# Performance work log

Hardware: AMD Instinct MI355X
Metric: run time of the kernel (lower is better)

The kernel has to match this reference:

```python
import jax, jax.numpy as jnp
import numpy as np

T, B, C, H, W = 4, 8, 256, 16, 16
HEADS = 8
N = H * W
TN = T * N
DH = C // HEADS
DECAY = 0.25

# STE quantizer: fwd round(clamp(x,0,1)); bwd passes grad only where 0<=x<=1
@jax.custom_vjp
def quant1(x):
    return jnp.round(jnp.clip(x, 0.0, 1.0))

def _q_fwd(x):
    return quant1(x), x

def _q_bwd(x, g):
    return (jnp.where((x < 0) | (x > 1), 0.0, g),)

quant1.defvjp(_q_fwd, _q_bwd)

def lif(x):
    # x: [T, ...]; sequential LIF membrane decay + quantize over leading (time) axis
    def step(carry, xt):
        mem_old, spike = carry
        mem = (mem_old - jax.lax.stop_gradient(spike) * 0.5) * DECAY + xt
        s = quant1(mem)
        return (mem, s), s
    z = jnp.zeros_like(x[0])
    _, out = jax.lax.scan(step, (z, z), x)
    return out

def bn1d(x, gamma, beta, mean, var):
    # eval-mode BatchNorm1d over channel axis 1 of [B, Ch, L]
    inv = jax.lax.rsqrt(var + 1e-5)
    return (x - mean[None, :, None]) * (gamma * inv)[None, :, None] + beta[None, :, None]

def _rel_pos_index():
    coords = np.stack(np.meshgrid(np.arange(T), np.arange(H), np.arange(W), indexing='ij'))  # [3,T,H,W]
    cf = coords.reshape(3, -1)                      # [3, TN]
    rc = (cf[:, :, None] - cf[:, None, :]).transpose(1, 2, 0).copy()  # [TN, TN, 3]
    rc[:, :, 0] += T - 1
    rc[:, :, 1] += H - 1
    rc[:, :, 2] += W - 1
    rc[:, :, 0] *= (2 * H - 1) * (2 * W - 1)
    rc[:, :, 1] *= (2 * W - 1)
    return rc.sum(-1)                               # [TN, TN] ints

def _mask():
    m = np.ones((TN, TN), np.float32)
    for t in range(T - 1):
        m[t * N:(t + 1) * N, (t + 1) * N:] = 0.0
    return m

_RPI = jnp.asarray(_rel_pos_index().reshape(-1))
_MASK = jnp.asarray(_mask())


def setup_inputs() -> dict:
    key = jax.random.key(0)
    ks = jax.random.split(key, 13)
    bias_rows = (2 * T - 1) * (2 * H - 1) * (2 * W - 1)
    return {
        'x': jax.random.normal(ks[0], (T, B, C, H, W), jnp.float32),
        'w_qkv': jax.random.normal(ks[1], (3 * C, C), jnp.float32) * 0.05,
        'qkv_gamma': jax.random.uniform(ks[2], (3 * C,), jnp.float32, 0.5, 1.5),
        'qkv_beta': jax.random.normal(ks[3], (3 * C,), jnp.float32) * 0.1,
        'qkv_mean': jax.random.normal(ks[4], (3 * C,), jnp.float32) * 0.1,
        'qkv_var': jax.random.uniform(ks[5], (3 * C,), jnp.float32, 0.5, 1.5),
        'bias_table': jax.random.normal(ks[6], (bias_rows, HEADS), jnp.float32) * 0.02,
        'w_proj': jax.random.normal(ks[7], (C, C), jnp.float32) * 0.05,
        'b_proj': jax.random.normal(ks[8], (C,), jnp.float32) * 0.02,
        'proj_gamma': jax.random.uniform(ks[9], (C,), jnp.float32, 0.5, 1.5),
        'proj_beta': jax.random.normal(ks[10], (C,), jnp.float32) * 0.1,
        'proj_mean': jax.random.normal(ks[11], (C,), jnp.float32) * 0.1,
        'proj_var': jax.random.uniform(ks[12], (C,), jnp.float32, 0.5, 1.5),
    }


def reference(x, w_qkv, qkv_gamma, qkv_beta, qkv_mean, qkv_var, bias_table,
              w_proj, b_proj, proj_gamma, proj_beta, proj_mean, proj_var):
    # flatten spatial, then raw reshape [T,B,C,N] -> [B,C,T*N] (as in torch source)
    xf = x.reshape(T, B, C, N).reshape(B, C, T * N)
    # 1x1 conv == channel matmul, then eval BN
    qkv = jnp.einsum('oc,bcl->bol', w_qkv, xf)
    qkv = bn1d(qkv, qkv_gamma, qkv_beta, qkv_mean, qkv_var)
    qkv = qkv.reshape(B, 3 * C, T, N).transpose(2, 0, 1, 3)  # [T,B,3C,N]
    qkv = lif(qkv).transpose(1, 0, 3, 2)                      # [B,T,N,3C]
    q, k, v = jnp.split(qkv, 3, axis=-1)                      # each [B,T,N,C]

    def to_heads(z):  # b t n (h d) -> b h (t n) d
        return z.reshape(B, T, N, HEADS, DH).transpose(0, 3, 1, 2, 4).reshape(B, HEADS, TN, DH)
    q, k, v = map(to_heads, (q, k, v))

    bias = bias_table[_RPI].reshape(TN, TN, HEADS).transpose(2, 0, 1)  # [h,TN,TN]
    attn = jnp.einsum('bhnd,bhmd->bhnm', q, k) + bias[None]
    attn = attn * _MASK[None, None]                                     # block upper-triangle mask
    o = jnp.einsum('bhnm,bhmd->bhnd', attn, v) * 0.125                  # [B,h,TN,d]

    o = o.transpose(0, 2, 1, 3).reshape(B, TN, C).reshape(B, T, N, C).transpose(1, 0, 3, 2)  # [T,B,C,N]
    o = lif(o)
    o = o.transpose(1, 2, 0, 3).reshape(B, C, T * N)          # [B,C,TN]
    o = jnp.einsum('oc,bcl->bol', w_proj, o) + b_proj[None, :, None]
    o = bn1d(o, proj_gamma, proj_beta, proj_mean, proj_var)
    o = o.reshape(B, C, T, N).transpose(2, 0, 1, 3).reshape(T, B, C, H, W)
    return lif(o)
```

## Files before the change

### kernel.cpp

```cpp
#include <hip/hip_runtime.h>
#include <stdint.h>
#include <math.h>

constexpr int T_ = 4;
constexpr int B_ = 8;
constexpr int C_ = 256;
constexpr int N_ = 256;
constexpr int TN_ = 1024;
constexpr int NH_ = 8;
constexpr int O3_ = 768;
constexpr int BIAS_ROWS_ = 6727;
constexpr int BCOL_P_ = 6784;

__device__ __constant__ int TI_OF[10] = {0,1,1,2,2,2,3,3,3,3};
__device__ __constant__ int TJ_OF[10] = {0,0,1,0,1,2,0,1,2,3};

__device__ __forceinline__ float quant1f(float m) {
    return rintf(fminf(fmaxf(m, 0.0f), 1.0f));
}

__global__ __launch_bounds__(256) void k0_bcol(
    const float* __restrict__ bias_table, float* __restrict__ bcol)
{
    const int idx = blockIdx.x * 256 + threadIdx.x;
    if (idx >= NH_ * BCOL_P_) return;
    const int h = idx / BCOL_P_, r = idx % BCOL_P_;
    bcol[idx] = (r < BIAS_ROWS_) ? bias_table[(size_t)r * NH_ + h] : 0.0f;
}

__global__ __launch_bounds__(256) void k1_qkv_gemm(
    const float* __restrict__ x, const float* __restrict__ w,
    const float* __restrict__ gamma, const float* __restrict__ beta,
    const float* __restrict__ mean, const float* __restrict__ var,
    float* __restrict__ out)
{
    __shared__ float At[16][100];
    __shared__ float Bt[16][132];
    const int b = blockIdx.z;
    const int oBase = blockIdx.y * 96;
    const int lBase = blockIdx.x * 128;
    const int tid = threadIdx.x;
    const int tx = tid & 31;
    const int ty = tid >> 5;
    const float* xb = x + (size_t)b * C_ * TN_;

    float acc[12][4];
#pragma unroll
    for (int i = 0; i < 12; ++i)
#pragma unroll
        for (int j = 0; j < 4; ++j) acc[i][j] = 0.0f;

    const int b_kk = tid >> 4, b_c4 = (tid & 15) * 4;

    for (int kc = 0; kc < 16; ++kc) {
        const int k0 = kc * 16;
#pragma unroll
        for (int r = 0; r < 3; ++r) {
            const int q = tid + 256 * r;
            const int row = q >> 3, k2 = (q & 7) * 2;
            const float2 v = *(const float2*)&w[(size_t)(oBase + row) * C_ + k0 + k2];
            At[k2][row] = v.x;
            At[k2 + 1][row] = v.y;
        }
#pragma unroll
        for (int r = 0; r < 2; ++r) {
            const float4 v = *(const float4*)&xb[(size_t)(k0 + b_kk) * TN_ + lBase + b_c4 + 64 * r];
            *(float4*)&Bt[b_kk][b_c4 + 64 * r] = v;
        }
        __syncthreads();
#pragma unroll
        for (int cc = 0; cc < 16; ++cc) {
            float a[12], bb[4];
            *(float4*)&a[0] = *(const float4*)&At[cc][ty * 4];
            *(float4*)&a[4] = *(const float4*)&At[cc][32 + ty * 4];
            *(float4*)&a[8] = *(const float4*)&At[cc][64 + ty * 4];
            *(float4*)&bb[0] = *(const float4*)&Bt[cc][tx * 4];
#pragma unroll
            for (int i = 0; i < 12; ++i)
#pragma unroll
                for (int j = 0; j < 4; ++j) acc[i][j] += a[i] * bb[j];
        }
        __syncthreads();
    }

#pragma unroll
    for (int i = 0; i < 12; ++i) {
        const int o = oBase + (i >> 2) * 32 + ty * 4 + (i & 3);
        const float inv = 1.0f / sqrtf(var[o] + 1e-5f);
        const float g = gamma[o] * inv;
        const float mn = mean[o], bt = beta[o];
        float4 st;
        st.x = (acc[i][0] - mn) * g + bt;
        st.y = (acc[i][1] - mn) * g + bt;
        st.z = (acc[i][2] - mn) * g + bt;
        st.w = (acc[i][3] - mn) * g + bt;
        *(float4*)&out[((size_t)b * O3_ + o) * TN_ + lBase + tx * 4] = st;
    }
}

__global__ __launch_bounds__(256) void k2_lif_pack(
    const float* __restrict__ qkv,
    uint32_t* __restrict__ qb, uint32_t* __restrict__ kb, uint32_t* __restrict__ vb)
{
    const int n = threadIdx.x;
    const int g = blockIdx.x;
    const int b = blockIdx.y;
    const int which = g >> 3, h = g & 7;
    uint32_t* dst = (which == 0) ? qb : (which == 1) ? kb : vb;
    const float* src = qkv + ((size_t)b * O3_ + g * 32) * TN_;

    float memv[32];
#pragma unroll
    for (int d = 0; d < 32; ++d) memv[d] = 0.0f;
    uint32_t prev = 0;

    for (int t = 0; t < T_; ++t) {
        uint32_t bits = 0;
#pragma unroll
        for (int d = 0; d < 32; ++d) {
            const float xv = src[(size_t)d * TN_ + t * N_ + n];
            const float m = (memv[d] - 0.5f * (float)((prev >> d) & 1u)) * 0.25f + xv;
            memv[d] = m;
            const float s = quant1f(m);
            bits |= ((uint32_t)s) << d;
        }
        prev = bits;
        dst[((size_t)b * NH_ + h) * TN_ + t * N_ + n] = bits;
    }
}

__global__ __launch_bounds__(256) void k3_transpose(
    const uint32_t* __restrict__ kb, const uint32_t* __restrict__ vb,
    uint64_t* __restrict__ ksel, uint64_t* __restrict__ vsel)
{
    const int t = blockIdx.x;
    const int h = blockIdx.y;
    const int b = blockIdx.z;
    const int bh = b * NH_ + h;
    const int tid = threadIdx.x;
    const int q = tid >> 6, lane = tid & 63;
    const int j = t * N_ + q * 64 + lane;

    const uint32_t kw = kb[(size_t)bh * TN_ + j];
    const uint32_t vw = vb[(size_t)bh * TN_ + j];
#pragma unroll
    for (int d = 0; d < 32; ++d) {
        const uint64_t mk = __ballot((kw >> d) & 1u);
        const uint64_t mv = __ballot((vw >> d) & 1u);
        if (lane == 0) {
            ksel[((size_t)(bh * 4 + t) * 32 + d) * 4 + q] = mk;
            vsel[((size_t)(bh * 4 + t) * 32 + d) * 4 + q] = mv;
        }
    }
}

__global__ __launch_bounds__(256) void k3_gram(
    const uint64_t* __restrict__ ksel, const uint64_t* __restrict__ vsel,
    float* __restrict__ Gf)
{
    const int bh = blockIdx.x;
    const int tid = threadIdx.x;
    const int d = tid & 31;
#pragma unroll
    for (int s = 0; s < 4; ++s) {
        const int d2 = (tid >> 5) + 8 * s;
        int cum = 0;
#pragma unroll
        for (int t = 0; t < T_; ++t) {
            const uint64_t* kp = ksel + ((size_t)(bh * 4 + t) * 32 + d2) * 4;
            const uint64_t* vp = vsel + ((size_t)(bh * 4 + t) * 32 + d) * 4;
            int p = 0;
#pragma unroll
            for (int w = 0; w < 4; ++w) p += __popcll(kp[w] & vp[w]);
            cum += p;
            Gf[(size_t)(bh * 4 + t) * 1024 + d2 * 32 + d] = (float)cum;
        }
    }
}

__global__ __launch_bounds__(256) void k3_s1(
    const uint32_t* __restrict__ qb, const float* __restrict__ Gf,
    float* __restrict__ oatt)
{
    __shared__ float sG[1024];
    const int ti = blockIdx.x;
    const int h = blockIdx.y;
    const int b = blockIdx.z;
    const int bh = b * NH_ + h;
    const int tid = threadIdx.x;
    const int d = tid & 31;

    for (int idx = tid; idx < 1024; idx += 256)
        sG[idx] = Gf[(size_t)(bh * 4 + ti) * 1024 + idx];
    __syncthreads();

    const uint32_t* qbh = qb + (size_t)bh * TN_;
    for (int step = 0; step < 32; ++step) {
        const int i = ti * N_ + step * 8 + (tid >> 5);
        const uint32_t q = qbh[i];
        float acc = 0.0f;
#pragma unroll
        for (int d2 = 0; d2 < 32; ++d2)
            acc += ((q >> d2) & 1u) ? sG[d2 * 32 + d] : 0.0f;
        oatt[((size_t)b * TN_ + i) * C_ + h * 32 + d] = acc;
    }
}

__global__ __launch_bounds__(256) void k3_bias_gemm(
    const uint32_t* __restrict__ vb, const float* __restrict__ bcol,
    float* __restrict__ p0, float* __restrict__ p1,
    float* __restrict__ p2, float* __restrict__ p3)
{
    __shared__ float sbl[640];
    __shared__ float Bt[16][64];

    const int z = blockIdx.z;
    const int h = z / 10;
    const int p = z % 10;
    const int ti = TI_OF[p], tj = TJ_OF[p];
    const int dt = ti - tj;
    const int iTile = blockIdx.y;
    const int nBase = blockIdx.x * 64;
    const int tid = threadIdx.x;

    const int base = 3363 + 961 * dt + 124 * iTile - 480;
    const float* bch = bcol + h * BCOL_P_;
    for (int s = tid; s < 640; s += 256) sbl[s] = bch[base + s];

    const int ty = tid >> 4, tx = tid & 15;
    const int ii0 = ty * 4;
    const int hi = (iTile * 64 + ii0) >> 4;
    const int wi0 = ii0 & 15;
    const int L0 = 31 * hi + wi0 - 124 * iTile + 480;

    const int ccb = tid >> 4;
    const int nb = nBase + (tid & 15) * 4;
    const int d0 = nb & 31;
    const uint32_t* vbw = vb + (((size_t)(nb >> 5)) * NH_ + h) * TN_ + tj * 256 + ccb;

    float acc[4][4];
#pragma unroll
    for (int i = 0; i < 4; ++i)
#pragma unroll
        for (int j = 0; j < 4; ++j) acc[i][j] = 0.0f;

    __syncthreads();

    for (int kc = 0; kc < 16; ++kc) {
        {
            const uint32_t w = vbw[kc * 16];
            float4 bv;
            bv.x = (float)((w >> d0) & 1u);
            bv.y = (float)((w >> (d0 + 1)) & 1u);
            bv.z = (float)((w >> (d0 + 2)) & 1u);
            bv.w = (float)((w >> (d0 + 3)) & 1u);
            *(float4*)&Bt[ccb][(tid & 15) * 4] = bv;
        }
        __syncthreads();
        const int aBase = L0 - 31 * kc;
#pragma unroll
        for (int cc = 0; cc < 16; ++cc) {
            const float a0 = sbl[aBase - cc];
            const float a1 = sbl[aBase - cc + 1];
            const float a2 = sbl[aBase - cc + 2];
            const float a3 = sbl[aBase - cc + 3];
            const float4 bx = *(const float4*)&Bt[cc][tx * 4];
            acc[0][0] += a0 * bx.x; acc[0][1] += a0 * bx.y; acc[0][2] += a0 * bx.z; acc[0][3] += a0 * bx.w;
            acc[1][0] += a1 * bx.x; acc[1][1] += a1 * bx.y; acc[1][2] += a1 * bx.z; acc[1][3] += a1 * bx.w;
            acc[2][0] += a2 * bx.x; acc[2][1] += a2 * bx.y; acc[2][2] += a2 * bx.z; acc[2][3] += a2 * bx.w;
            acc[3][0] += a3 * bx.x; acc[3][1] += a3 * bx.y; acc[3][2] += a3 * bx.z; acc[3][3] += a3 * bx.w;
        }
        __syncthreads();
    }

    float* plane = (tj == 0) ? p0 : (tj == 1) ? p1 : (tj == 2) ? p2 : p3;
    const int nrows = (4 - tj) * 256;
    const int bb = nb >> 5;
    const int c0 = h * 32 + d0;
#pragma unroll
    for (int r = 0; r < 4; ++r) {
        const int rowL = dt * 256 + iTile * 64 + ii0 + r;
        float4 st;
        st.x = acc[r][0]; st.y = acc[r][1]; st.z = acc[r][2]; st.w = acc[r][3];
        *(float4*)&plane[((size_t)bb * nrows + rowL) * 256 + c0] = st;
    }
}

__global__ __launch_bounds__(256) void k4_lif2(
    const float* __restrict__ oatt,
    const float* __restrict__ p0, const float* __restrict__ p1,
    const float* __restrict__ p2, const float* __restrict__ p3,
    uint32_t* __restrict__ s2c)
{
    const int c = threadIdx.x;
    const int n = blockIdx.x;
    const int b = blockIdx.y;
    const int lane = c & 63;
    float memv = 0.0f, spk = 0.0f;
    for (int t = 0; t < T_; ++t) {
        const int l = t * N_ + n;
        float v = oatt[((size_t)b * TN_ + l) * C_ + c];
        v += p0[((size_t)b * 1024 + l) * 256 + c];
        if (t >= 1) v += p1[((size_t)b * 768 + (l - 256)) * 256 + c];
        if (t >= 2) v += p2[((size_t)b * 512 + (l - 512)) * 256 + c];
        if (t >= 3) v += p3[((size_t)b * 256 + (l - 768)) * 256 + c];
        const float m = (memv - 0.5f * spk) * 0.25f + 0.125f * v;
        memv = m;
        const float s = quant1f(m);
        spk = s;
        const uint64_t mask = __ballot(s != 0.0f);
        if (lane == 0)
            s2c[((size_t)b * TN_ + l) * 8 + (c >> 5)] = (uint32_t)mask;
        else if (lane == 32)
            s2c[((size_t)b * TN_ + l) * 8 + (c >> 5)] = (uint32_t)(mask >> 32);
    }
}

__global__ __launch_bounds__(256) void k5_proj_gemm(
    const uint32_t* __restrict__ s2c, const float* __restrict__ w,
    const float* __restrict__ bp,
    const float* __restrict__ gamma, const float* __restrict__ beta,
    const float* __restrict__ mean, const float* __restrict__ var,
    float* __restrict__ pbn)
{
    __shared__ float At[16][36];
    __shared__ float Bt[16][132];
    const int b = blockIdx.z;
    const int oBase = blockIdx.y * 32;
    const int lBase = blockIdx.x * 128;
    const int tid = threadIdx.x;
    const int tx = tid & 31;
    const int ty = tid >> 5;

    const int a_row = tid >> 3, a_k2 = (tid & 7) * 2;
    const int b_ll = tid >> 1, b_sub = tid & 1;
    const uint32_t* srow = s2c + ((size_t)b * TN_ + lBase + b_ll) * 8;

    float acc[4][4];
#pragma unroll
    for (int i = 0; i < 4; ++i)
#pragma unroll
        for (int j = 0; j < 4; ++j) acc[i][j] = 0.0f;

    for (int kc = 0; kc < 16; ++kc) {
        const int k0 = kc * 16;
        {
            const float2 v = *(const float2*)&w[(size_t)(oBase + a_row) * C_ + k0 + a_k2];
            At[a_k2][a_row] = v.x;
            At[a_k2 + 1][a_row] = v.y;
        }
        {
            const uint32_t wd = srow[kc >> 1];
            const int sh = ((kc & 1) << 4) + (b_sub << 3);
#pragma unroll
            for (int u = 0; u < 8; ++u)
                Bt[(b_sub << 3) + u][b_ll] = (float)((wd >> (sh + u)) & 1u);
        }
        __syncthreads();
#pragma unroll
        for (int cc = 0; cc < 16; ++cc) {
            float a[4], bb[4];
            *(float4*)&a[0] = *(const float4*)&At[cc][ty * 4];
            *(float4*)&bb[0] = *(const float4*)&Bt[cc][tx * 4];
#pragma unroll
            for (int i = 0; i < 4; ++i)
#pragma unroll
                for (int j = 0; j < 4; ++j) acc[i][j] += a[i] * bb[j];
        }
        __syncthreads();
    }

#pragma unroll
    for (int i = 0; i < 4; ++i) {
        const int o = oBase + ty * 4 + i;
        const float inv = 1.0f / sqrtf(var[o] + 1e-5f);
        const float g = gamma[o] * inv;
        const float mn = mean[o], bt = beta[o], bpo = bp[o];
        float4 st;
        st.x = ((acc[i][0] + bpo) - mn) * g + bt;
        st.y = ((acc[i][1] + bpo) - mn) * g + bt;
        st.z = ((acc[i][2] + bpo) - mn) * g + bt;
        st.w = ((acc[i][3] + bpo) - mn) * g + bt;
        *(float4*)&pbn[((size_t)b * C_ + o) * TN_ + lBase + tx * 4] = st;
    }
}

__global__ __launch_bounds__(256) void k6_lif3(
    const float* __restrict__ pbn, float* __restrict__ out)
{
    const int n = threadIdx.x;
    const int c = blockIdx.x;
    const int b = blockIdx.y;
    const float* src = pbn + ((size_t)b * C_ + c) * TN_;
    float memv = 0.0f, spk = 0.0f;
    for (int t = 0; t < T_; ++t) {
        const float m = (memv - 0.5f * spk) * 0.25f + src[t * N_ + n];
        memv = m;
        const float s = quant1f(m);
        out[(((size_t)t * B_ + b) * C_ + c) * N_ + n] = s;
        spk = s;
    }
}

extern "C" void kernel_launch(void* const* d_in, const int* in_sizes, int n_in,
                              void* d_out, int out_size, void* d_ws, size_t ws_size,
                              hipStream_t stream)
{
    const float* x          = (const float*)d_in[0];
    const float* w_qkv      = (const float*)d_in[1];
    const float* qkv_gamma  = (const float*)d_in[2];
    const float* qkv_beta   = (const float*)d_in[3];
    const float* qkv_mean   = (const float*)d_in[4];
    const float* qkv_var    = (const float*)d_in[5];
    const float* bias_table = (const float*)d_in[6];
    const float* w_proj     = (const float*)d_in[7];
    const float* b_proj     = (const float*)d_in[8];
    const float* proj_gamma = (const float*)d_in[9];
    const float* proj_beta  = (const float*)d_in[10];
    const float* proj_mean  = (const float*)d_in[11];
    const float* proj_var   = (const float*)d_in[12];
    float* out = (float*)d_out;

    char* ws = (char*)d_ws;
    float*    qkv_bn = (float*)(ws + 0);
    uint64_t* ksel   = (uint64_t*)(ws + 0);
    uint64_t* vsel   = (uint64_t*)(ws + 262144);
    float*    Gf     = (float*)(ws + 524288);
    float*    part0  = (float*)(ws + 1048576);
    float*    part1  = (float*)(ws + 9437184);
    float*    part2  = (float*)(ws + 15728640);
    float*    part3  = (float*)(ws + 19922944);
    float*    oatt   = (float*)(ws + 25165824);
    uint32_t* s2c    = (uint32_t*)(ws + 33554432);
    float*    pbn    = (float*)(ws + 41943040);
    uint32_t* qbits  = (uint32_t*)(ws + 50331648);
    uint32_t* kbits  = (uint32_t*)(ws + 50593792);
    uint32_t* vbits  = (uint32_t*)(ws + 50855936);
    float*    bcol   = (float*)(ws + 51118080);

    k0_bcol<<<dim3((NH_ * BCOL_P_ + 255) / 256), 256, 0, stream>>>(bias_table, bcol);

    k1_qkv_gemm<<<dim3(8, 8, 8), 256, 0, stream>>>(
        x, w_qkv, qkv_gamma, qkv_beta, qkv_mean, qkv_var, qkv_bn);

    k2_lif_pack<<<dim3(24, 8), 256, 0, stream>>>(qkv_bn, qbits, kbits, vbits);

    k3_transpose<<<dim3(4, 8, 8), 256, 0, stream>>>(kbits, vbits, ksel, vsel);

    k3_gram<<<dim3(64), 256, 0, stream>>>(ksel, vsel, Gf);

    k3_s1<<<dim3(4, 8, 8), 256, 0, stream>>>(qbits, Gf, oatt);

    k3_bias_gemm<<<dim3(4, 4, 80), 256, 0, stream>>>(
        vbits, bcol, part0, part1, part2, part3);

    k4_lif2<<<dim3(256, 8), 256, 0, stream>>>(oatt, part0, part1, part2, part3, s2c);

    k5_proj_gemm<<<dim3(8, 8, 8), 256, 0, stream>>>(
        s2c, w_proj, b_proj, proj_gamma, proj_beta, proj_mean, proj_var, pbn);

    k6_lif3<<<dim3(256, 8), 256, 0, stream>>>(pbn, out);
}
```

Before: 244.7 us.

## Double-buffer QKV GEMM, register-cache Gram in s1, widen bias GEMM tiles

The QKV GEMM now prefetches the next k-slice into registers and writes it into a second shared-memory buffer, so global loads overlap compute and one barrier per iteration goes away. k3_s1 keeps the per-column Gram values in registers instead of shared memory and launches four times as many blocks, each covering a quarter of the rows. k3_bias_gemm stages the Toeplitz bias slice into an At tile and uses a 4x8 register tile over 128 columns, halving its grid. The cost is more shared memory and registers, which may lower occupancy.

```diff
diff --git a/kernel.cpp b/kernel.cpp
--- a/kernel.cpp
+++ b/kernel.cpp
@@ -34,8 +34,8 @@
     const float* __restrict__ mean, const float* __restrict__ var,
     float* __restrict__ out)
 {
-    __shared__ float At[16][100];
-    __shared__ float Bt[16][132];
+    __shared__ float At[2][16][100];
+    __shared__ float Bt[2][16][132];
     const int b = blockIdx.z;
     const int oBase = blockIdx.y * 96;
     const int lBase = blockIdx.x * 128;
@@ -51,36 +51,68 @@
         for (int j = 0; j < 4; ++j) acc[i][j] = 0.0f;
 
     const int b_kk = tid >> 4, b_c4 = (tid & 15) * 4;
+    int a_row[3], a_k2[3];
+#pragma unroll
+    for (int r = 0; r < 3; ++r) {
+        const int q = tid + 256 * r;
+        a_row[r] = q >> 3;
+        a_k2[r] = (q & 7) * 2;
+    }
+
+    float2 aReg[3];
+    float4 bReg[2];
+
+#pragma unroll
+    for (int r = 0; r < 3; ++r)
+        aReg[r] = *(const float2*)&w[(size_t)(oBase + a_row[r]) * C_ + a_k2[r]];
+#pragma unroll
+    for (int r = 0; r < 2; ++r)
+        bReg[r] = *(const float4*)&xb[(size_t)b_kk * TN_ + lBase + b_c4 + 64 * r];
+#pragma unroll
+    for (int r = 0; r < 3; ++r) {
+        At[0][a_k2[r]][a_row[r]] = aReg[r].x;
+        At[0][a_k2[r] + 1][a_row[r]] = aReg[r].y;
+    }
+#pragma unroll
+    for (int r = 0; r < 2; ++r)
+        *(float4*)&Bt[0][b_kk][b_c4 + 64 * r] = bReg[r];
+    __syncthreads();
 
     for (int kc = 0; kc < 16; ++kc) {
-        const int k0 = kc * 16;
-#pragma unroll
-        for (int r = 0; r < 3; ++r) {
-            const int q = tid + 256 * r;
-            const int row = q >> 3, k2 = (q & 7) * 2;
-            const float2 v = *(const float2*)&w[(size_t)(oBase + row) * C_ + k0 + k2];
-            At[k2][row] = v.x;
-            At[k2 + 1][row] = v.y;
-        }
-#pragma unroll
-        for (int r = 0; r < 2; ++r) {
-            const float4 v = *(const float4*)&xb[(size_t)(k0 + b_kk) * TN_ + lBase + b_c4 + 64 * r];
-            *(float4*)&Bt[b_kk][b_c4 + 64 * r] = v;
-        }
-        __syncthreads();
+        const int buf = kc & 1;
+        if (kc < 15) {
+            const int k0 = (kc + 1) * 16;
+#pragma unroll
+            for (int r = 0; r < 3; ++r)
+                aReg[r] = *(const float2*)&w[(size_t)(oBase + a_row[r]) * C_ + k0 + a_k2[r]];
+#pragma unroll
+            for (int r = 0; r < 2; ++r)
+                bReg[r] = *(const float4*)&xb[(size_t)(k0 + b_kk) * TN_ + lBase + b_c4 + 64 * r];
+        }
 #pragma unroll
         for (int cc = 0; cc < 16; ++cc) {
             float a[12], bb[4];
-            *(float4*)&a[0] = *(const float4*)&At[cc][ty * 4];
-            *(float4*)&a[4] = *(const float4*)&At[cc][32 + ty * 4];
-            *(float4*)&a[8] = *(const float4*)&At[cc][64 + ty * 4];
-            *(float4*)&bb[0] = *(const float4*)&Bt[cc][tx * 4];
+            *(float4*)&a[0] = *(const float4*)&At[buf][cc][ty * 4];
+            *(float4*)&a[4] = *(const float4*)&At[buf][cc][32 + ty * 4];
+            *(float4*)&a[8] = *(const float4*)&At[buf][cc][64 + ty * 4];
+            *(float4*)&bb[0] = *(const float4*)&Bt[buf][cc][tx * 4];
 #pragma unroll
             for (int i = 0; i < 12; ++i)
 #pragma unroll
                 for (int j = 0; j < 4; ++j) acc[i][j] += a[i] * bb[j];
         }
-        __syncthreads();
+        if (kc < 15) {
+            const int nb = buf ^ 1;
+#pragma unroll
+            for (int r = 0; r < 3; ++r) {
+                At[nb][a_k2[r]][a_row[r]] = aReg[r].x;
+                At[nb][a_k2[r] + 1][a_row[r]] = aReg[r].y;
+            }
+#pragma unroll
+            for (int r = 0; r < 2; ++r)
+                *(float4*)&Bt[nb][b_kk][b_c4 + 64 * r] = bReg[r];
+            __syncthreads();
+        }
     }
 
 #pragma unroll
@@ -182,26 +214,30 @@
     const uint32_t* __restrict__ qb, const float* __restrict__ Gf,
     float* __restrict__ oatt)
 {
-    __shared__ float sG[1024];
-    const int ti = blockIdx.x;
+    const int grp = blockIdx.x;
+    const int ti = grp >> 2, seg = grp & 3;
     const int h = blockIdx.y;
     const int b = blockIdx.z;
     const int bh = b * NH_ + h;
     const int tid = threadIdx.x;
     const int d = tid & 31;
-
-    for (int idx = tid; idx < 1024; idx += 256)
-        sG[idx] = Gf[(size_t)(bh * 4 + ti) * 1024 + idx];
-    __syncthreads();
+    const int ig = tid >> 5;
+
+    const float* gsrc = Gf + (size_t)(bh * 4 + ti) * 1024 + d;
+    float g[32];
+#pragma unroll
+    for (int d2 = 0; d2 < 32; ++d2) g[d2] = gsrc[d2 * 32];
 
     const uint32_t* qbh = qb + (size_t)bh * TN_;
-    for (int step = 0; step < 32; ++step) {
-        const int i = ti * N_ + step * 8 + (tid >> 5);
+    const int i0 = ti * N_ + seg * 64 + ig * 8;
+#pragma unroll
+    for (int s = 0; s < 8; ++s) {
+        const int i = i0 + s;
         const uint32_t q = qbh[i];
         float acc = 0.0f;
 #pragma unroll
         for (int d2 = 0; d2 < 32; ++d2)
-            acc += ((q >> d2) & 1u) ? sG[d2 * 32 + d] : 0.0f;
+            acc += ((q >> d2) & 1u) ? g[d2] : 0.0f;
         oatt[((size_t)b * TN_ + i) * C_ + h * 32 + d] = acc;
     }
 }
@@ -212,77 +248,93 @@
     float* __restrict__ p2, float* __restrict__ p3)
 {
     __shared__ float sbl[640];
-    __shared__ float Bt[16][64];
+    __shared__ float At[16][68];
+    __shared__ float Bt[16][132];
 
     const int z = blockIdx.z;
     const int h = z / 10;
     const int p = z % 10;
     const int ti = TI_OF[p], tj = TJ_OF[p];
     const int dt = ti - tj;
-    const int iTile = blockIdx.y;
-    const int nBase = blockIdx.x * 64;
+    const int iT = blockIdx.y;
+    const int nBase = blockIdx.x * 128;
     const int tid = threadIdx.x;
 
-    const int base = 3363 + 961 * dt + 124 * iTile - 480;
+    const int base = 3363 + 961 * dt + 124 * iT - 480;
     const float* bch = bcol + h * BCOL_P_;
     for (int s = tid; s < 640; s += 256) sbl[s] = bch[base + s];
 
     const int ty = tid >> 4, tx = tid & 15;
-    const int ii0 = ty * 4;
-    const int hi = (iTile * 64 + ii0) >> 4;
-    const int wi0 = ii0 & 15;
-    const int L0 = 31 * hi + wi0 - 124 * iTile + 480;
-
-    const int ccb = tid >> 4;
-    const int nb = nBase + (tid & 15) * 4;
-    const int d0 = nb & 31;
-    const uint32_t* vbw = vb + (((size_t)(nb >> 5)) * NH_ + h) * TN_ + tj * 256 + ccb;
-
-    float acc[4][4];
+
+    const int ccS = tx;
+    const int iBase4 = ty * 4;
+    const int sIdxBase = 31 * (iBase4 >> 4) + (iBase4 & 15) + 480 - ccS;
+
+    const int kkS = ty;
+    const int n8 = tx * 8;
+    const int nS = nBase + n8;
+    const int bS = nS >> 5, d0S = nS & 31;
+    const uint32_t* vbw = vb + ((size_t)bS * NH_ + h) * TN_ + tj * 256 + kkS;
+
+    float acc[4][8];
 #pragma unroll
     for (int i = 0; i < 4; ++i)
 #pragma unroll
-        for (int j = 0; j < 4; ++j) acc[i][j] = 0.0f;
+        for (int j = 0; j < 8; ++j) acc[i][j] = 0.0f;
 
     __syncthreads();
 
     for (int kc = 0; kc < 16; ++kc) {
         {
-            const uint32_t w = vbw[kc * 16];
-            float4 bv;
-            bv.x = (float)((w >> d0) & 1u);
-            bv.y = (float)((w >> (d0 + 1)) & 1u);
-            bv.z = (float)((w >> (d0 + 2)) & 1u);
-            bv.w = (float)((w >> (d0 + 3)) & 1u);
-            *(float4*)&Bt[ccb][(tid & 15) * 4] = bv;
+            const int s0 = sIdxBase - 31 * kc;
+            float4 av;
+            av.x = sbl[s0];
+            av.y = sbl[s0 + 1];
+            av.z = sbl[s0 + 2];
+            av.w = sbl[s0 + 3];
+            *(float4*)&At[ccS][iBase4] = av;
+        }
+        {
+            const uint32_t wd = vbw[kc * 16];
+            float4 b0, b1;
+            b0.x = (float)((wd >> d0S) & 1u);
+            b0.y = (float)((wd >> (d0S + 1)) & 1u);
+            b0.z = (float)((wd >> (d0S + 2)) & 1u);
+            b0.w = (float)((wd >> (d0S + 3)) & 1u);
+            b1.x = (float)((wd >> (d0S + 4)) & 1u);
+            b1.y = (float)((wd >> (d0S + 5)) & 1u);
+            b1.z = (float)((wd >> (d0S + 6)) & 1u);
+            b1.w = (float)((wd >> (d0S + 7)) & 1u);
+            *(float4*)&Bt[kkS][n8] = b0;
+            *(float4*)&Bt[kkS][n8 + 4] = b1;
         }
         __syncthreads();
-        const int aBase = L0 - 31 * kc;
 #pragma unroll
         for (int cc = 0; cc < 16; ++cc) {
-            const float a0 = sbl[aBase - cc];
-            const float a1 = sbl[aBase - cc + 1];
-            const float a2 = sbl[aBase - cc + 2];
-            const float a3 = sbl[aBase - cc + 3];
-            const float4 bx = *(const float4*)&Bt[cc][tx * 4];
-            acc[0][0] += a0 * bx.x; acc[0][1] += a0 * bx.y; acc[0][2] += a0 * bx.z; acc[0][3] += a0 * bx.w;
-            acc[1][0] += a1 * bx.x; acc[1][1] += a1 * bx.y; acc[1][2] += a1 * bx.z; acc[1][3] += a1 * bx.w;
-            acc[2][0] += a2 * bx.x; acc[2][1] += a2 * bx.y; acc[2][2] += a2 * bx.z; acc[2][3] += a2 * bx.w;
-            acc[3][0] += a3 * bx.x; acc[3][1] += a3 * bx.y; acc[3][2] += a3 * bx.z; acc[3][3] += a3 * bx.w;
+            float a[4], bb[8];
+            *(float4*)&a[0] = *(const float4*)&At[cc][ty * 4];
+            *(float4*)&bb[0] = *(const float4*)&Bt[cc][tx * 8];
+            *(float4*)&bb[4] = *(const float4*)&Bt[cc][tx * 8 + 4];
+#pragma unroll
+            for (int i = 0; i < 4; ++i)
+#pragma unroll
+                for (int j = 0; j < 8; ++j) acc[i][j] += a[i] * bb[j];
         }
         __syncthreads();
     }
 
     float* plane = (tj == 0) ? p0 : (tj == 1) ? p1 : (tj == 2) ? p2 : p3;
     const int nrows = (4 - tj) * 256;
-    const int bb = nb >> 5;
-    const int c0 = h * 32 + d0;
+    const int c0 = h * 32 + d0S;
 #pragma unroll
     for (int r = 0; r < 4; ++r) {
-        const int rowL = dt * 256 + iTile * 64 + ii0 + r;
-        float4 st;
-        st.x = acc[r][0]; st.y = acc[r][1]; st.z = acc[r][2]; st.w = acc[r][3];
-        *(float4*)&plane[((size_t)bb * nrows + rowL) * 256 + c0] = st;
+        const int rowL = dt * 256 + iT * 64 + ty * 4 + r;
+        float* dst = &plane[((size_t)bS * nrows + rowL) * 256 + c0];
+        float4 s0, s1;
+        s0.x = acc[r][0]; s0.y = acc[r][1]; s0.z = acc[r][2]; s0.w = acc[r][3];
+        s1.x = acc[r][4]; s1.y = acc[r][5]; s1.z = acc[r][6]; s1.w = acc[r][7];
+        *(float4*)&dst[0] = s0;
+        *(float4*)&dst[4] = s1;
     }
 }
 
@@ -449,9 +501,9 @@
 
     k3_gram<<<dim3(64), 256, 0, stream>>>(ksel, vsel, Gf);
 
-    k3_s1<<<dim3(4, 8, 8), 256, 0, stream>>>(qbits, Gf, oatt);
-
-    k3_bias_gemm<<<dim3(4, 4, 80), 256, 0, stream>>>(
+    k3_s1<<<dim3(16, 8, 8), 256, 0, stream>>>(qbits, Gf, oatt);
+
+    k3_bias_gemm<<<dim3(2, 4, 80), 256, 0, stream>>>(
         vbits, bcol, part0, part1, part2, part3);
 
     k4_lif2<<<dim3(256, 8), 256, 0, stream>>>(oatt, part0, part1, part2, part3, s2c);
```

New measurement: 261.5 us. 6.9% more time.
